# Optimization experiments

Hardware: AMD Instinct MI355X
Metric: run time of the kernel (lower is better)

The kernel has to match this reference:

```python
import jax, jax.numpy as jnp
import numpy as np

D_MODEL = 1024
NUM_HEADS = 16
D_HEAD = D_MODEL // NUM_HEADS
MAX_LEN = 16384
BATCH = 4
SEQ = 1024


def setup_inputs() -> dict:
    key = jax.random.key(0)
    ks = jax.random.split(key, 10)
    s = 1.0 / np.sqrt(D_MODEL)
    return {
        "q_in": jax.random.normal(ks[0], (BATCH, SEQ, D_MODEL), jnp.float32),
        "k_in": jax.random.normal(ks[1], (BATCH, SEQ, D_MODEL), jnp.float32),
        "v_in": jax.random.normal(ks[2], (BATCH, SEQ, D_MODEL), jnp.float32),
        "Wq": jax.random.normal(ks[3], (D_MODEL, D_MODEL), jnp.float32) * s,
        "bq": jnp.zeros((D_MODEL,), jnp.float32),
        "Wk": jax.random.normal(ks[4], (D_MODEL, D_MODEL), jnp.float32) * s,
        "bk": jnp.zeros((D_MODEL,), jnp.float32),
        "Wv": jax.random.normal(ks[5], (D_MODEL, D_MODEL), jnp.float32) * s,
        "bv": jnp.zeros((D_MODEL,), jnp.float32),
        "Er": jax.random.normal(ks[6], (MAX_LEN, D_HEAD), jnp.float32),
    }


def _skew(QEr):
    # QEr: [B, H, S, S] -> pad one zero column on the left, reshape, drop row 0
    B, H, S, _ = QEr.shape
    padded = jnp.pad(QEr, ((0, 0), (0, 0), (0, 0), (1, 0)))  # [B,H,S,S+1]
    reshaped = padded.reshape(B, H, S + 1, S)
    return reshaped[:, :, 1:, :]  # [B,H,S,S]


def reference(q_in, k_in, v_in, Wq, bq, Wk, bk, Wv, bv, Er):
    B, S, _ = q_in.shape
    H, Dh = NUM_HEADS, D_HEAD
    # projections, split into heads: [B, H, S, Dh]
    q = (q_in @ Wq + bq).reshape(B, S, H, Dh).transpose(0, 2, 1, 3)
    k = (k_in @ Wk + bk).reshape(B, S, H, Dh).transpose(0, 2, 1, 3)
    v = (v_in @ Wv + bv).reshape(B, S, H, Dh).transpose(0, 2, 1, 3)
    # relative position scores: Er slice [S, Dh]
    Er_sl = Er[MAX_LEN - S:, :]
    QEr = jnp.einsum('bhsd,td->bhst', q, Er_sl)  # [B,H,S,S]
    Srel = _skew(QEr)
    QK = jnp.einsum('bhsd,bhtd->bhst', q, k)
    attn = (QK + Srel) / jnp.sqrt(jnp.asarray(Dh, q.dtype))
    attn = jax.nn.softmax(attn, axis=-1)
    out = jnp.einsum('bhst,bhtd->bhsd', attn, v)  # [B,H,S,Dh]
    out = out.transpose(0, 2, 1, 3).reshape(B, S, H * Dh)
    return out
```

## Files before the change

kernel.cpp:

```cpp
#include <hip/hip_runtime.h>
#include <hip/hip_bf16.h>
#include <cstdint>

#define S_LEN 1024
#define DMODEL 1024
#define NHEADS 16
#define DHEAD 64
#define MAXLEN 16384
#define BATCH 4

typedef __attribute__((ext_vector_type(8))) short bf16x8;
typedef __attribute__((ext_vector_type(4))) float f32x4;

#define AS1(p) ((const __attribute__((address_space(1))) unsigned int*)(p))
#define AS3(p) ((__attribute__((address_space(3))) unsigned int*)(p))

__device__ inline unsigned short f2b(float f) {
  unsigned int u = __float_as_uint(f);
  unsigned int r = (u + 0x7FFFu + ((u >> 16) & 1u)) >> 16;
  return (unsigned short)r;
}
__device__ inline float b2f(unsigned short u) {
  return __uint_as_float(((unsigned int)u) << 16);
}

#define LDSWZ(row, slot) (((row) << 6) + (((slot) ^ ((row) & 7)) << 3))

__global__ __launch_bounds__(256) void wt_er_convert(
    const float* __restrict__ W0, const float* __restrict__ W1, const float* __restrict__ W2,
    unsigned short* __restrict__ T0, unsigned short* __restrict__ T1, unsigned short* __restrict__ T2,
    const float* __restrict__ Er, unsigned short* __restrict__ Erb) {
  const int z = blockIdx.z;
  if (z == 3) {
    const int o = blockIdx.y * 32 + blockIdx.x;
    if (o < 64) {
      const int i = o * 1024 + threadIdx.x * 4;
      float4 f = *(const float4*)(Er + (size_t)(MAXLEN - S_LEN) * DHEAD + i);
      Erb[i] = f2b(f.x); Erb[i + 1] = f2b(f.y);
      Erb[i + 2] = f2b(f.z); Erb[i + 3] = f2b(f.w);
    }
    return;
  }
  const float* W = (z == 0) ? W0 : (z == 1) ? W1 : W2;
  unsigned short* WT = (z == 0) ? T0 : (z == 1) ? T1 : T2;
  __shared__ float t[32][33];
  const int bi = blockIdx.y * 32, bj = blockIdx.x * 32;
  const int r = threadIdx.x >> 3, c4 = (threadIdx.x & 7) * 4;
  float4 f = *(const float4*)&W[(size_t)(bi + r) * DMODEL + bj + c4];
  t[r][c4] = f.x; t[r][c4 + 1] = f.y; t[r][c4 + 2] = f.z; t[r][c4 + 3] = f.w;
  __syncthreads();
  ushort4 u;
  u.x = f2b(t[c4][r]); u.y = f2b(t[c4 + 1][r]);
  u.z = f2b(t[c4 + 2][r]); u.w = f2b(t[c4 + 3][r]);
  *(ushort4*)&WT[(size_t)(bj + r) * DMODEL + bi + c4] = u;
}

__global__ __launch_bounds__(256) void xconvert3(
    const float* __restrict__ X0, const float* __restrict__ X1, const float* __restrict__ X2,
    unsigned short* __restrict__ B0, unsigned short* __restrict__ B1, unsigned short* __restrict__ B2) {
  const int z = blockIdx.z;
  const float* X = (z == 0) ? X0 : (z == 1) ? X1 : X2;
  unsigned short* B = (z == 0) ? B0 : (z == 1) ? B1 : B2;
  size_t i = ((size_t)blockIdx.x * 256 + threadIdx.x) * 16;
  union { unsigned short h[16]; int4 v[2]; } u;
#pragma unroll
  for (int r = 0; r < 4; ++r) {
    float4 f = *(const float4*)(X + i + r * 4);
    u.h[r * 4 + 0] = f2b(f.x); u.h[r * 4 + 1] = f2b(f.y);
    u.h[r * 4 + 2] = f2b(f.z); u.h[r * 4 + 3] = f2b(f.w);
  }
  *(int4*)(B + i) = u.v[0];
  *(int4*)(B + i + 8) = u.v[1];
}

__global__ __launch_bounds__(256) void proj_glds3(
    const unsigned short* __restrict__ Xq, const unsigned short* __restrict__ Xk,
    const unsigned short* __restrict__ Xv,
    const unsigned short* __restrict__ T0, const unsigned short* __restrict__ T1,
    const unsigned short* __restrict__ T2,
    const float* __restrict__ b0, const float* __restrict__ b1, const float* __restrict__ b2,
    unsigned short* __restrict__ O0, unsigned short* __restrict__ O1,
    unsigned short* __restrict__ O2) {
  const int z = blockIdx.z;
  const unsigned short* X = (z == 0) ? Xq : (z == 1) ? Xk : Xv;
  const unsigned short* WT = (z == 0) ? T0 : (z == 1) ? T1 : T2;
  const float* bias = (z == 0) ? b0 : (z == 1) ? b1 : b2;
  unsigned short* Out = (z == 0) ? O0 : (z == 1) ? O1 : O2;
  const float osc = (z == 0) ? 0.125f : 1.0f;
  __shared__ unsigned short As[128 * 64];
  __shared__ unsigned short Bs[128 * 64];
  const int tid = threadIdx.x;
  const int l = tid & 63, w = tid >> 6;
  const int o = blockIdx.y * 8 + blockIdx.x;
  const int lid = (o & 7) * 32 + (o >> 3);
  const int bm = (lid >> 3) * 128, bn = (lid & 7) * 128;
  const int wr = (w >> 1) * 64, wc = (w & 1) * 64;
  const int lrow = l >> 3;
  const int slotlog = (l & 7) ^ (lrow & 7);
  const unsigned short* Xa = X + (size_t)(bm + lrow) * DMODEL + slotlog * 8;
  const unsigned short* Wa = WT + (size_t)(bn + lrow) * DMODEL + slotlog * 8;
  f32x4 acc[4][4] = {};
  for (int k0 = 0; k0 < DMODEL; k0 += 64) {
    __syncthreads();
#pragma unroll
    for (int j = 0; j < 4; ++j) {
      int r8 = (w * 4 + j) * 8;
      __builtin_amdgcn_global_load_lds(AS1(Xa + (size_t)r8 * DMODEL + k0),
                                       AS3(&As[(w * 4 + j) * 512]), 16, 0, 0);
      __builtin_amdgcn_global_load_lds(AS1(Wa + (size_t)r8 * DMODEL + k0),
                                       AS3(&Bs[(w * 4 + j) * 512]), 16, 0, 0);
    }
    __syncthreads();
#pragma unroll
    for (int ks = 0; ks < 2; ++ks) {
      bf16x8 a[4], b[4];
#pragma unroll
      for (int f = 0; f < 4; ++f) {
        int row = wr + f * 16 + (l & 15);
        a[f] = *(const bf16x8*)&As[LDSWZ(row, ks * 4 + (l >> 4))];
        int col = wc + f * 16 + (l & 15);
        b[f] = *(const bf16x8*)&Bs[LDSWZ(col, ks * 4 + (l >> 4))];
      }
#pragma unroll
      for (int i = 0; i < 4; ++i)
#pragma unroll
        for (int j = 0; j < 4; ++j)
          acc[i][j] = __builtin_amdgcn_mfma_f32_16x16x32_bf16(a[i], b[j], acc[i][j], 0, 0, 0);
    }
  }
#pragma unroll
  for (int i = 0; i < 4; ++i) {
    int m = bm + wr + i * 16 + ((l >> 4) << 2);
#pragma unroll
    for (int j = 0; j < 4; ++j) {
      int n = bn + wc + j * 16 + (l & 15);
      float bv = bias[n];
#pragma unroll
      for (int e = 0; e < 4; ++e)
        Out[(size_t)(m + e) * DMODEL + n] = f2b((acc[i][j][e] + bv) * osc);
    }
  }
}

__global__ __launch_bounds__(256) void qer_mfma(const unsigned short* __restrict__ qp,
    const unsigned short* __restrict__ Erb, unsigned short* __restrict__ G, int bh0) {
  const int bh = bh0 + blockIdx.z;
  const int b = bh >> 4, h = bh & 15;
  __shared__ unsigned short As[128 * 64];
  __shared__ unsigned short Bs[128 * 64];
  const int tid = threadIdx.x, l = tid & 63, wid = tid >> 6;
  const int bm = blockIdx.y * 128, bn = blockIdx.x * 128;
  const int wr = (wid >> 1) * 64, wc = (wid & 1) * 64;
  const unsigned short* qb = qp + (size_t)b * S_LEN * DMODEL + h * DHEAD;
  unsigned short* Gc = G + (size_t)blockIdx.z * S_LEN * S_LEN;
#pragma unroll
  for (int r = 0; r < 4; ++r) {
    int s = r * 256 + tid;
    int row = s >> 3, sl = s & 7;
    *(int4*)&As[LDSWZ(row, sl)] = *(const int4*)(qb + (size_t)(bm + row) * DMODEL + sl * 8);
    *(int4*)&Bs[LDSWZ(row, sl)] = *(const int4*)(Erb + (size_t)(bn + row) * DHEAD + sl * 8);
  }
  if (blockIdx.x == 0 && tid < 128) {
    int s = bm + tid;
    if (s < S_LEN - 1) Gc[(size_t)s * S_LEN + s + 1] = 0;
  }
  __syncthreads();
  f32x4 acc[4][4] = {};
#pragma unroll
  for (int ks = 0; ks < 2; ++ks) {
    bf16x8 a[4], b[4];
#pragma unroll
    for (int f = 0; f < 4; ++f) {
      int row = wr + f * 16 + (l & 15);
      a[f] = *(const bf16x8*)&As[LDSWZ(row, ks * 4 + (l >> 4))];
      int col = wc + f * 16 + (l & 15);
      b[f] = *(const bf16x8*)&Bs[LDSWZ(col, ks * 4 + (l >> 4))];
    }
#pragma unroll
    for (int i = 0; i < 4; ++i)
#pragma unroll
      for (int j = 0; j < 4; ++j)
        acc[i][j] = __builtin_amdgcn_mfma_f32_16x16x32_bf16(a[i], b[j], acc[i][j], 0, 0, 0);
  }
#pragma unroll
  for (int i = 0; i < 4; ++i) {
    int m = bm + wr + i * 16 + ((l >> 4) << 2);
#pragma unroll
    for (int j = 0; j < 4; ++j) {
      int n = bn + wc + j * 16 + (l & 15);
#pragma unroll
      for (int e = 0; e < 4; ++e) {
        int s = m + e;
        int hi = (n >= 1023 - s);
        int r_ = hi ? s : s - 1;
        int t_ = hi ? (n + s - 1023) : (n + s + 1);
        if (r_ >= 0)
          Gc[(size_t)r_ * S_LEN + t_] = f2b(acc[i][j][e]);
      }
    }
  }
}

__global__ __launch_bounds__(256) void attn_skew(const unsigned short* __restrict__ qp,
    const unsigned short* __restrict__ kp, const unsigned short* __restrict__ vp,
    const unsigned short* __restrict__ G, float* __restrict__ out, int bh0) {
  const int bh = bh0 + blockIdx.y;
  const int b = bh >> 4, h = bh & 15;
  const int s0 = blockIdx.x * 64;
  __shared__ unsigned short Qs[64 * 64];
  __shared__ unsigned short Ks[64 * 64];
  __shared__ unsigned short Vt[64 * 64];
  __shared__ unsigned short Ps[4][16 * 64];
  const int tid = threadIdx.x, l = tid & 63, w = tid >> 6;
  const int lg = l >> 4, li = l & 15;
  const unsigned short* qb = qp + (size_t)b * S_LEN * DMODEL + h * DHEAD;
  const unsigned short* kb = kp + (size_t)b * S_LEN * DMODEL + h * DHEAD;
  const unsigned short* vb = vp + (size_t)b * S_LEN * DMODEL + h * DHEAD;
  const unsigned short* Gb = G + (size_t)blockIdx.y * S_LEN * S_LEN;

#pragma unroll
  for (int r = 0; r < 2; ++r) {
    int s = r * 256 + tid;
    int row = s >> 3, sl = s & 7;
    *(int4*)&Qs[LDSWZ(row, sl)] = *(const int4*)(qb + (size_t)(s0 + row) * DMODEL + sl * 8);
  }
  __syncthreads();
  bf16x8 qf[2];
#pragma unroll
  for (int ks = 0; ks < 2; ++ks)
    qf[ks] = *(const bf16x8*)&Qs[LDSWZ(w * 16 + li, ks * 4 + lg)];

  f32x4 o4[4] = {};
  float lsum[4] = {0.f, 0.f, 0.f, 0.f};
  int sg[4];
  const unsigned short* gp[4];
#pragma unroll
  for (int i = 0; i < 4; ++i) {
    sg[i] = s0 + w * 16 + (lg << 2) + i;
    gp[i] = Gb + (size_t)sg[i] * S_LEN + li;
  }
  const int pr = tid & 31, dh0 = (tid >> 5) * 8;
  const float L2E = 1.44269504f;
  const float SHF = 16.f * 1.44269504f;

  for (int ti = 0; ti < 16; ++ti) {
    const int t0 = ti * 64;
    __syncthreads();
#pragma unroll
    for (int r = 0; r < 2; ++r) {
      int s = r * 256 + tid; int row = s >> 3, sl = s & 7;
      *(int4*)&Ks[LDSWZ(row, sl)] = *(const int4*)(kb + (size_t)(t0 + row) * DMODEL + sl * 8);
    }
    {
      const unsigned short* v0p = vb + (size_t)(t0 + pr * 2) * DMODEL + dh0;
      union { int4 v; unsigned short hh[8]; } va, vc;
      va.v = *(const int4*)v0p;
      vc.v = *(const int4*)(v0p + DMODEL);
      unsigned int* vtw = (unsigned int*)Vt;
#pragma unroll
      for (int j = 0; j < 8; ++j) {
        int dh = dh0 + j;
        int widx = dh * 32 + (((pr >> 2) ^ (dh & 7)) << 2) + (pr & 3);
        vtw[widx] = (unsigned int)va.hh[j] | ((unsigned int)vc.hh[j] << 16);
      }
    }
    __syncthreads();
    unsigned short rv[4][4];
#pragma unroll
    for (int f = 0; f < 4; ++f)
#pragma unroll
      for (int i = 0; i < 4; ++i)
        rv[f][i] = gp[i][t0 + f * 16];
    f32x4 sa[4] = {};
#pragma unroll
    for (int ks = 0; ks < 2; ++ks)
#pragma unroll
      for (int f = 0; f < 4; ++f) {
        bf16x8 kf = *(const bf16x8*)&Ks[LDSWZ(f * 16 + li, ks * 4 + lg)];
        sa[f] = __builtin_amdgcn_mfma_f32_16x16x32_bf16(qf[ks], kf, sa[f], 0, 0, 0);
      }
    unsigned short* Pw = &Ps[w][0];
#pragma unroll
    for (int f = 0; f < 4; ++f) {
#pragma unroll
      for (int i = 0; i < 4; ++i) {
        float sv = sa[f][i] + b2f(rv[f][i]);
        float pv = __builtin_exp2f(__builtin_fmaf(sv, L2E, -SHF));
        unsigned int pu = __float_as_uint(pv) & 0xffff0000u;
        lsum[i] += __uint_as_float(pu);
        int prow = (lg << 2) + i, pcol = f * 16 + li;
        Pw[LDSWZ(prow, pcol >> 3) + (pcol & 7)] = (unsigned short)(pu >> 16);
      }
    }
#pragma unroll
    for (int ks = 0; ks < 2; ++ks) {
      bf16x8 pf = *(const bf16x8*)&Pw[LDSWZ(li, ks * 4 + lg)];
#pragma unroll
      for (int f = 0; f < 4; ++f) {
        bf16x8 vf = *(const bf16x8*)&Vt[LDSWZ(f * 16 + li, ks * 4 + lg)];
        o4[f] = __builtin_amdgcn_mfma_f32_16x16x32_bf16(pf, vf, o4[f], 0, 0, 0);
      }
    }
  }
#pragma unroll
  for (int off = 8; off >= 1; off >>= 1)
#pragma unroll
    for (int i = 0; i < 4; ++i) lsum[i] += __shfl_xor(lsum[i], off);
#pragma unroll
  for (int i = 0; i < 4; ++i) {
    float inv = 1.f / lsum[i];
#pragma unroll
    for (int f = 0; f < 4; ++f)
      out[(size_t)(b * S_LEN + sg[i]) * DMODEL + h * DHEAD + f * 16 + li] = o4[f][i] * inv;
  }
}

extern "C" void kernel_launch(void* const* d_in, const int* in_sizes, int n_in,
                              void* d_out, int out_size, void* d_ws, size_t ws_size,
                              hipStream_t stream) {
  (void)in_sizes; (void)n_in; (void)out_size;
  const float* q_in = (const float*)d_in[0];
  const float* k_in = (const float*)d_in[1];
  const float* v_in = (const float*)d_in[2];
  const float* Wq   = (const float*)d_in[3];
  const float* bq   = (const float*)d_in[4];
  const float* Wk   = (const float*)d_in[5];
  const float* bk   = (const float*)d_in[6];
  const float* Wv   = (const float*)d_in[7];
  const float* bv   = (const float*)d_in[8];
  const float* Er   = (const float*)d_in[9];
  float* out = (float*)d_out;

  char* ws = (char*)d_ws;
  const size_t MB = (size_t)1 << 20;
  unsigned short* wtq = (unsigned short*)(ws);
  unsigned short* wtk = (unsigned short*)(ws + 2 * MB);
  unsigned short* wtv = (unsigned short*)(ws + 4 * MB);
  unsigned short* erb = (unsigned short*)(ws + 6 * MB);
  unsigned short* qp  = (unsigned short*)(ws + 8 * MB);
  unsigned short* kp  = (unsigned short*)(ws + 16 * MB);
  unsigned short* vp  = (unsigned short*)(ws + 24 * MB);
  unsigned short* xq  = (unsigned short*)(ws + 32 * MB);
  unsigned short* xk  = (unsigned short*)(ws + 40 * MB);
  unsigned short* xv  = (unsigned short*)(ws + 48 * MB);
  unsigned short* G   = (unsigned short*)(ws + 56 * MB);

  const size_t gavail = (ws_size > 56 * MB) ? (ws_size - 56 * MB) : 0;
  int chunk = (int)(gavail / (2 * MB));
  if (chunk < 1) chunk = 1;
  if (chunk > 64) chunk = 64;

  dim3 blk(256);
  hipLaunchKernelGGL(wt_er_convert, dim3(32, 32, 4), blk, 0, stream,
                     Wq, Wk, Wv, wtq, wtk, wtv, Er, erb);
  hipLaunchKernelGGL(xconvert3, dim3(1024, 1, 3), blk, 0, stream,
                     q_in, k_in, v_in, xq, xk, xv);

  dim3 gproj(DMODEL / 128, (BATCH * S_LEN) / 128, 3);
  hipLaunchKernelGGL(proj_glds3, gproj, blk, 0, stream,
                     xq, xk, xv, wtq, wtk, wtv, bq, bk, bv, qp, kp, vp);

  for (int bh0 = 0; bh0 < BATCH * NHEADS; bh0 += chunk) {
    int nb = BATCH * NHEADS - bh0;
    if (nb > chunk) nb = chunk;
    dim3 gqer(S_LEN / 128, S_LEN / 128, nb);
    hipLaunchKernelGGL(qer_mfma, gqer, blk, 0, stream, qp, erb, G, bh0);
    dim3 gattn(S_LEN / 64, nb);
    hipLaunchKernelGGL(attn_skew, gattn, blk, 0, stream, qp, kp, vp, G, out, bh0);
  }
}
```

Baseline: 165.0 us.

## Split attention over key halves and combine partials in separate kernel

Splits each attention block's key range into two halves processed by separate workgroups, doubling grid size, then adds a combine kernel that sums the partial outputs and row sums and normalizes. Because softmax uses a fixed shift instead of a running max, the partials can simply be added. LDS is also merged into one buffer, with the P scratch reusing the Q staging area, which cuts shared memory per block. The cost is an extra launch, writing and re-reading fp32 partials, and 33MB less workspace available for G chunks.

```diff
diff --git a/kernel.cpp b/kernel.cpp
--- a/kernel.cpp
+++ b/kernel.cpp
@@ -201,62 +201,63 @@
   }
 }
 
-__global__ __launch_bounds__(256) void attn_skew(const unsigned short* __restrict__ qp,
+__global__ __launch_bounds__(256) void attn_split(const unsigned short* __restrict__ qp,
     const unsigned short* __restrict__ kp, const unsigned short* __restrict__ vp,
-    const unsigned short* __restrict__ G, float* __restrict__ out, int bh0) {
-  const int bh = bh0 + blockIdx.y;
+    const unsigned short* __restrict__ G, float* __restrict__ Opart,
+    float* __restrict__ lpart, int bh0) {
+  const int bhl = blockIdx.y;
+  const int bh = bh0 + bhl;
   const int b = bh >> 4, h = bh & 15;
-  const int s0 = blockIdx.x * 64;
-  __shared__ unsigned short Qs[64 * 64];
-  __shared__ unsigned short Ks[64 * 64];
-  __shared__ unsigned short Vt[64 * 64];
-  __shared__ unsigned short Ps[4][16 * 64];
+  const int sblk = blockIdx.x >> 1, half = blockIdx.x & 1;
+  const int s0 = sblk * 64;
+  __shared__ unsigned short lds[12288];
+  const int KS = 0, VT = 4096, QP = 8192;
   const int tid = threadIdx.x, l = tid & 63, w = tid >> 6;
   const int lg = l >> 4, li = l & 15;
   const unsigned short* qb = qp + (size_t)b * S_LEN * DMODEL + h * DHEAD;
   const unsigned short* kb = kp + (size_t)b * S_LEN * DMODEL + h * DHEAD;
   const unsigned short* vb = vp + (size_t)b * S_LEN * DMODEL + h * DHEAD;
-  const unsigned short* Gb = G + (size_t)blockIdx.y * S_LEN * S_LEN;
+  const unsigned short* Gb = G + (size_t)bhl * S_LEN * S_LEN;
 
 #pragma unroll
   for (int r = 0; r < 2; ++r) {
     int s = r * 256 + tid;
     int row = s >> 3, sl = s & 7;
-    *(int4*)&Qs[LDSWZ(row, sl)] = *(const int4*)(qb + (size_t)(s0 + row) * DMODEL + sl * 8);
+    *(int4*)&lds[QP + LDSWZ(row, sl)] =
+        *(const int4*)(qb + (size_t)(s0 + row) * DMODEL + sl * 8);
   }
   __syncthreads();
   bf16x8 qf[2];
 #pragma unroll
   for (int ks = 0; ks < 2; ++ks)
-    qf[ks] = *(const bf16x8*)&Qs[LDSWZ(w * 16 + li, ks * 4 + lg)];
+    qf[ks] = *(const bf16x8*)&lds[QP + LDSWZ(w * 16 + li, ks * 4 + lg)];
 
   f32x4 o4[4] = {};
   float lsum[4] = {0.f, 0.f, 0.f, 0.f};
-  int sg[4];
   const unsigned short* gp[4];
 #pragma unroll
-  for (int i = 0; i < 4; ++i) {
-    sg[i] = s0 + w * 16 + (lg << 2) + i;
-    gp[i] = Gb + (size_t)sg[i] * S_LEN + li;
-  }
+  for (int i = 0; i < 4; ++i)
+    gp[i] = Gb + (size_t)(s0 + w * 16 + (lg << 2) + i) * S_LEN + li;
   const int pr = tid & 31, dh0 = (tid >> 5) * 8;
   const float L2E = 1.44269504f;
   const float SHF = 16.f * 1.44269504f;
 
-  for (int ti = 0; ti < 16; ++ti) {
+  const int tiEnd = half * 8 + 8;
+  for (int ti = half * 8; ti < tiEnd; ++ti) {
     const int t0 = ti * 64;
     __syncthreads();
 #pragma unroll
     for (int r = 0; r < 2; ++r) {
       int s = r * 256 + tid; int row = s >> 3, sl = s & 7;
-      *(int4*)&Ks[LDSWZ(row, sl)] = *(const int4*)(kb + (size_t)(t0 + row) * DMODEL + sl * 8);
+      *(int4*)&lds[KS + LDSWZ(row, sl)] =
+          *(const int4*)(kb + (size_t)(t0 + row) * DMODEL + sl * 8);
     }
     {
       const unsigned short* v0p = vb + (size_t)(t0 + pr * 2) * DMODEL + dh0;
       union { int4 v; unsigned short hh[8]; } va, vc;
       va.v = *(const int4*)v0p;
       vc.v = *(const int4*)(v0p + DMODEL);
-      unsigned int* vtw = (unsigned int*)Vt;
+      unsigned int* vtw = (unsigned int*)(lds + VT);
 #pragma unroll
       for (int j = 0; j < 8; ++j) {
         int dh = dh0 + j;
@@ -276,10 +277,10 @@
     for (int ks = 0; ks < 2; ++ks)
 #pragma unroll
       for (int f = 0; f < 4; ++f) {
-        bf16x8 kf = *(const bf16x8*)&Ks[LDSWZ(f * 16 + li, ks * 4 + lg)];
+        bf16x8 kf = *(const bf16x8*)&lds[KS + LDSWZ(f * 16 + li, ks * 4 + lg)];
         sa[f] = __builtin_amdgcn_mfma_f32_16x16x32_bf16(qf[ks], kf, sa[f], 0, 0, 0);
       }
-    unsigned short* Pw = &Ps[w][0];
+    unsigned short* Pw = lds + QP + w * 1024;
 #pragma unroll
     for (int f = 0; f < 4; ++f) {
 #pragma unroll
@@ -297,7 +298,7 @@
       bf16x8 pf = *(const bf16x8*)&Pw[LDSWZ(li, ks * 4 + lg)];
 #pragma unroll
       for (int f = 0; f < 4; ++f) {
-        bf16x8 vf = *(const bf16x8*)&Vt[LDSWZ(f * 16 + li, ks * 4 + lg)];
+        bf16x8 vf = *(const bf16x8*)&lds[VT + LDSWZ(f * 16 + li, ks * 4 + lg)];
         o4[f] = __builtin_amdgcn_mfma_f32_16x16x32_bf16(pf, vf, o4[f], 0, 0, 0);
       }
     }
@@ -306,12 +307,41 @@
   for (int off = 8; off >= 1; off >>= 1)
 #pragma unroll
     for (int i = 0; i < 4; ++i) lsum[i] += __shfl_xor(lsum[i], off);
+  float* Ob = Opart + (((size_t)(bhl * 16 + sblk) * 2 + half) * 4096);
 #pragma unroll
   for (int i = 0; i < 4; ++i) {
-    float inv = 1.f / lsum[i];
+    int row = w * 16 + (lg << 2) + i;
 #pragma unroll
     for (int f = 0; f < 4; ++f)
-      out[(size_t)(b * S_LEN + sg[i]) * DMODEL + h * DHEAD + f * 16 + li] = o4[f][i] * inv;
+      Ob[row * 64 + f * 16 + li] = o4[f][i];
+  }
+  if (li == 0) {
+    float* lb = lpart + ((size_t)(bhl * 16 + sblk) * 2 + half) * 64;
+#pragma unroll
+    for (int i = 0; i < 4; ++i) lb[w * 16 + (lg << 2) + i] = lsum[i];
+  }
+}
+
+__global__ __launch_bounds__(256) void attn_combine(const float* __restrict__ Opart,
+    const float* __restrict__ lpart, float* __restrict__ out, int bh0) {
+  const int bhl = blockIdx.y, sblk = blockIdx.x;
+  const int bh = bh0 + bhl;
+  const int b = bh >> 4, h = bh & 15;
+  const int tid = threadIdx.x;
+  const int r = tid >> 2, c0 = (tid & 3) * 16;
+  const float* O1 = Opart + ((size_t)(bhl * 16 + sblk) * 2) * 4096;
+  const float* O2 = O1 + 4096;
+  const float* l1 = lpart + (size_t)(bhl * 16 + sblk) * 2 * 64;
+  const float inv = 1.f / (l1[r] + l1[64 + r]);
+  float* ob = out + (size_t)(b * S_LEN + sblk * 64 + r) * DMODEL + h * DHEAD + c0;
+#pragma unroll
+  for (int j = 0; j < 4; ++j) {
+    float4 a = *(const float4*)(O1 + r * 64 + c0 + j * 4);
+    float4 c = *(const float4*)(O2 + r * 64 + c0 + j * 4);
+    float4 wv;
+    wv.x = (a.x + c.x) * inv; wv.y = (a.y + c.y) * inv;
+    wv.z = (a.z + c.z) * inv; wv.w = (a.w + c.w) * inv;
+    *(float4*)(ob + j * 4) = wv;
   }
 }
 
@@ -343,9 +373,11 @@
   unsigned short* xq  = (unsigned short*)(ws + 32 * MB);
   unsigned short* xk  = (unsigned short*)(ws + 40 * MB);
   unsigned short* xv  = (unsigned short*)(ws + 48 * MB);
-  unsigned short* G   = (unsigned short*)(ws + 56 * MB);
-
-  const size_t gavail = (ws_size > 56 * MB) ? (ws_size - 56 * MB) : 0;
+  float* Opart = (float*)(ws + 56 * MB);
+  float* lpart = (float*)(ws + 88 * MB);
+  unsigned short* G = (unsigned short*)(ws + 89 * MB);
+
+  const size_t gavail = (ws_size > 89 * MB) ? (ws_size - 89 * MB) : 0;
   int chunk = (int)(gavail / (2 * MB));
   if (chunk < 1) chunk = 1;
   if (chunk > 64) chunk = 64;
@@ -365,7 +397,10 @@
     if (nb > chunk) nb = chunk;
     dim3 gqer(S_LEN / 128, S_LEN / 128, nb);
     hipLaunchKernelGGL(qer_mfma, gqer, blk, 0, stream, qp, erb, G, bh0);
-    dim3 gattn(S_LEN / 64, nb);
-    hipLaunchKernelGGL(attn_skew, gattn, blk, 0, stream, qp, kp, vp, G, out, bh0);
-  }
-}
+    dim3 gattn(32, nb);
+    hipLaunchKernelGGL(attn_split, gattn, blk, 0, stream, qp, kp, vp, G,
+                       Opart, lpart, bh0);
+    dim3 gcomb(16, nb);
+    hipLaunchKernelGGL(attn_combine, gcomb, blk, 0, stream, Opart, lpart, out, bh0);
+  }
+}
```

Result: slower. 174.6 us (+5.8%).
